# Kernel optimization log

Hardware: AMD Instinct MI355X
Metric: run time of the kernel (lower is better)

Reference implementation:

```python
import jax, jax.numpy as jnp
import numpy as np

N = 100_000      # nodes
E = 3_200_000    # directed edges (avg degree 32)
F_IN = 503
C = 32           # GATConv out_channels, heads=1
NEG_SLOPE = 0.2  # PyG GATConv default


def setup_inputs() -> dict:
    key = jax.random.key(0)
    ks = jax.random.split(key, 14)
    x = jax.random.normal(ks[0], (N, F_IN), jnp.float32)
    edge_index = jax.random.randint(ks[1], (2, E), 0, N)
    edge_weight = jax.random.uniform(ks[2], (E, 1), jnp.float32)
    input_mask = jnp.ones((N, 1), jnp.float32)
    # GATConv params (heads=1)
    W_src = jax.random.normal(ks[3], (C, F_IN), jnp.float32) * 0.02
    att_src = jax.random.normal(ks[4], (C,), jnp.float32) * 0.1
    att_dst = jax.random.normal(ks[5], (C,), jnp.float32) * 0.1
    att_edge = jax.random.normal(ks[6], (C,), jnp.float32) * 0.1
    W_edge = jax.random.normal(ks[7], (C, 1), jnp.float32) * 0.1
    bias_conv = jnp.zeros((C,), jnp.float32)
    # dense heads
    Wb = jax.random.normal(ks[8], (1, C), jnp.float32) * 0.1
    bb = jnp.zeros((1,), jnp.float32)
    Ww = jax.random.normal(ks[9], (1, C), jnp.float32) * 0.1
    bw = jnp.zeros((1,), jnp.float32)
    return {"x": x, "edge_index": edge_index, "edge_weight": edge_weight,
            "input_mask": input_mask, "W_src": W_src, "att_src": att_src,
            "att_dst": att_dst, "att_edge": att_edge, "W_edge": W_edge,
            "bias_conv": bias_conv, "Wb": Wb, "bb": bb, "Ww": Ww, "bw": bw}


def reference(x, edge_index, edge_weight, input_mask, W_src, att_src, att_dst,
              att_edge, W_edge, bias_conv, Wb, bb, Ww, bw):
    n = x.shape[0]
    xl = x @ W_src.T                       # [N, C] transformed node features
    a_src = xl @ att_src                   # [N] per-node source attention logit
    a_dst = xl @ att_dst                   # [N]
    src, dst = edge_index[0], edge_index[1]
    # add_self_loops=True with fill_value='mean' for edge_attr (PyG default)
    loop = jnp.arange(n)
    mean_attr = jnp.mean(edge_weight, axis=0, keepdims=True)      # [1,1]
    ea = jnp.concatenate([edge_weight, jnp.broadcast_to(mean_attr, (n, 1))], 0)
    s = jnp.concatenate([src, loop])       # [E+N]
    d = jnp.concatenate([dst, loop])
    a_edge = (ea @ W_edge.T) @ att_edge    # [E+N]
    alpha = jax.nn.leaky_relu(a_src[s] + a_dst[d] + a_edge, NEG_SLOPE)
    # softmax over incoming edges of each destination node
    amax = jax.ops.segment_max(alpha, d, num_segments=n)
    ex = jnp.exp(alpha - amax[d])
    denom = jax.ops.segment_sum(ex, d, num_segments=n)
    w = ex / denom[d]                      # [E+N] attention coeffs
    msg = xl[s] * w[:, None]               # [E+N, C]
    out = jax.ops.segment_sum(msg, d, num_segments=n) + bias_conv  # [N, C]
    h = jax.nn.relu(out)
    biases = (h @ Wb.T + bb) * input_mask  # [N, 1]
    weights = ((h[src] + h[dst]) * 0.5) @ Ww.T + bw  # [E, 1]
    return weights, biases
```

## Files before the change

kernel.cpp:

```cpp
#include <hip/hip_runtime.h>
#include <stdint.h>

#define NN 100000
#define NE 3200000
#define FIN 503
#define COUT 32
#define NSLOPE 0.2f

#define BSH 6
#define NB 1563
#define HB 256
#define EPB (NE / HB)
#define MAXBE 2400
#define NREG 10

typedef __bf16 bf16x8 __attribute__((ext_vector_type(8)));
typedef float  f32x4  __attribute__((ext_vector_type(4)));

__device__ __forceinline__ unsigned short bf1(float f) {
    unsigned u = __float_as_uint(f);
    u = (u + 0x7FFFu + ((u >> 16) & 1u)) >> 16;
    return (unsigned short)u;
}
__device__ __forceinline__ unsigned bf2(float a, float b) {
    return (unsigned)bf1(a) | ((unsigned)bf1(b) << 16);
}
__device__ __forceinline__ float unbf(unsigned short h) {
    return __uint_as_float(((unsigned)h) << 16);
}

__global__ __launch_bounds__(256)
void k_stats(const float* __restrict__ ew, float* __restrict__ partial,
             const float* __restrict__ W, uint4* __restrict__ wfrag)
{
    const int t = threadIdx.x;
    const int gid = blockIdx.x * 256 + t;

    if (gid < 2048) {
        int c = gid & 31;
        int quad = (gid >> 5) & 3;
        int chunk = gid >> 7;
        int kb = chunk * 32 + quad * 8;
        float v[8];
        #pragma unroll
        for (int j = 0; j < 8; ++j) {
            int k = kb + j;
            v[j] = (k < FIN) ? W[c * FIN + k] : 0.f;
        }
        uint4 o;
        o.x = bf2(v[0], v[1]); o.y = bf2(v[2], v[3]);
        o.z = bf2(v[4], v[5]); o.w = bf2(v[6], v[7]);
        wfrag[gid] = o;
    }

    const float4* ew4 = (const float4*)ew;
    float s = 0.f;
    for (int i = gid; i < NE / 4; i += gridDim.x * 256) {
        float4 v = ew4[i];
        s += v.x + v.y + v.z + v.w;
    }
    #pragma unroll
    for (int off = 32; off > 0; off >>= 1) s += __shfl_xor(s, off);
    __shared__ float wsum[4];
    if ((t & 63) == 0) wsum[t >> 6] = s;
    __syncthreads();
    if (t == 0) partial[blockIdx.x] = wsum[0] + wsum[1] + wsum[2] + wsum[3];
}

#define GR 64

__global__ __launch_bounds__(256)
void k_gemm(const float* __restrict__ x, const uint4* __restrict__ wfrag,
            const float* __restrict__ att_s, const float* __restrict__ att_d,
            unsigned short* __restrict__ xlb,
            float* __restrict__ a_src, float* __restrict__ a_dst)
{
    __shared__ __align__(16) float xs[GR][36];
    __shared__ __align__(16) unsigned short os[GR * 40];
    const int t = threadIdx.x;
    const int wv = t >> 6, lane = t & 63;
    const int m16 = lane & 15, quad = lane >> 4;
    const int row0 = blockIdx.x * GR;
    const int srow = t >> 5;
    const int scol = t & 31;

    f32x4 acc0 = {0.f, 0.f, 0.f, 0.f};
    f32x4 acc1 = {0.f, 0.f, 0.f, 0.f};
    const int rowf = wv * 16 + m16;

    for (int ch = 0; ch < 16; ++ch) {
        const int k = ch * 32 + scol;
        #pragma unroll
        for (int p = 0; p < 8; ++p) {
            int r = p * 8 + srow;
            int rg = row0 + r;
            rg = (rg < NN) ? rg : (NN - 1);
            xs[r][scol] = (k < FIN) ? x[(size_t)rg * FIN + k] : 0.f;
        }
        __syncthreads();
        float av[8];
        *(f32x4*)&av[0] = *(const f32x4*)&xs[rowf][quad * 8];
        *(f32x4*)&av[4] = *(const f32x4*)&xs[rowf][quad * 8 + 4];
        bf16x8 af;
        #pragma unroll
        for (int j = 0; j < 8; ++j) af[j] = (__bf16)av[j];
        uint4 b0 = wfrag[ch * 128 + quad * 32 + m16];
        uint4 b1 = wfrag[ch * 128 + quad * 32 + 16 + m16];
        acc0 = __builtin_amdgcn_mfma_f32_16x16x32_bf16(af, *(bf16x8*)&b0, acc0, 0, 0, 0);
        acc1 = __builtin_amdgcn_mfma_f32_16x16x32_bf16(af, *(bf16x8*)&b1, acc1, 0, 0, 0);
        __syncthreads();
    }

    #pragma unroll
    for (int r = 0; r < 4; ++r) {
        int rr = wv * 16 + quad * 4 + r;
        os[rr * 40 + m16]      = bf1(acc0[r]);
        os[rr * 40 + 16 + m16] = bf1(acc1[r]);
    }
    __syncthreads();
    {
        int r = t >> 2, c0 = (t & 3) * 8;
        int grow = row0 + r;
        uint4 o = *(const uint4*)&os[r * 40 + c0];
        float s = 0.f, dd = 0.f;
        const unsigned short* oh = (const unsigned short*)&o;
        #pragma unroll
        for (int j = 0; j < 8; ++j) {
            float v = unbf(oh[j]);
            s  += v * att_s[c0 + j];
            dd += v * att_d[c0 + j];
        }
        s  += __shfl_xor(s, 1, 4);  s  += __shfl_xor(s, 2, 4);
        dd += __shfl_xor(dd, 1, 4); dd += __shfl_xor(dd, 2, 4);
        if (grow < NN) {
            *(uint4*)&xlb[(size_t)grow * COUT + c0] = o;
            if ((t & 3) == 0) { a_src[grow] = s; a_dst[grow] = dd; }
        }
    }
}

__global__ __launch_bounds__(512)
void k_hist(const int* __restrict__ ei_dst, unsigned* __restrict__ part)
{
    __shared__ unsigned h[NB];
    for (int i = threadIdx.x; i < NB; i += 512) h[i] = 0u;
    __syncthreads();
    const int base = blockIdx.x * EPB;
    for (int i = threadIdx.x; i < EPB; i += 512)
        atomicAdd(&h[ei_dst[base + i] >> BSH], 1u);
    __syncthreads();
    for (int i = threadIdx.x; i < NB; i += 512)
        part[(size_t)blockIdx.x * NB + i] = h[i];
}

__global__ void k_colscan(unsigned* __restrict__ part, unsigned* __restrict__ colsum)
{
    __shared__ unsigned sm[HB];
    const int t = threadIdx.x;
    const int bkt = blockIdx.x;
    unsigned v = part[(size_t)t * NB + bkt];
    sm[t] = v;
    for (int off = 1; off < HB; off <<= 1) {
        __syncthreads();
        unsigned tv = (t >= off) ? sm[t - off] : 0u;
        __syncthreads();
        sm[t] += tv;
    }
    __syncthreads();
    part[(size_t)t * NB + bkt] = sm[t] - v;
    if (t == HB - 1) colsum[bkt] = sm[t];
}

__global__ void k_bscan(const unsigned* __restrict__ colsum, unsigned* __restrict__ bbase,
                        const float* __restrict__ partial, const float* __restrict__ W_edge,
                        const float* __restrict__ att_e, float* __restrict__ stats)
{
    const int t = threadIdx.x;
    {
        __shared__ float fs[256];
        float ps = partial[t] + partial[t + 256] + partial[t + 512] + partial[t + 768];
        fs[t] = ps;
        __syncthreads();
        for (int off = 128; off > 0; off >>= 1) {
            if (t < off) fs[t] += fs[t + off];
            __syncthreads();
        }
        if (t == 0) {
            stats[0] = fs[0];
            float k = 0.f;
            for (int c = 0; c < COUT; ++c) k += W_edge[c] * att_e[c];
            stats[1] = k;
        }
    }
    __syncthreads();

    __shared__ unsigned sm[256];
    __shared__ unsigned carry;
    if (t == 0) carry = 0u;
    __syncthreads();
    for (int c0 = 0; c0 < NB; c0 += 256) {
        int i = c0 + t;
        unsigned v = (i < NB) ? colsum[i] : 0u;
        sm[t] = v;
        for (int off = 1; off < 256; off <<= 1) {
            __syncthreads();
            unsigned tv = (t >= off) ? sm[t - off] : 0u;
            __syncthreads();
            sm[t] += tv;
        }
        __syncthreads();
        if (i < NB) bbase[i] = carry + sm[t] - v;
        __syncthreads();
        if (t == 0) carry += sm[255];
        __syncthreads();
    }
    if (t == 0) bbase[NB] = carry;
}

__global__ __launch_bounds__(512)
void k_scatter(const int* __restrict__ ei, const float* __restrict__ ew,
               const float* __restrict__ a_src, const float* __restrict__ stats,
               const unsigned* __restrict__ part, const unsigned* __restrict__ bbase,
               uint2* __restrict__ csr)
{
    __shared__ unsigned cur[NB];
    const int b = blockIdx.x;
    for (int i = threadIdx.x; i < NB; i += 512)
        cur[i] = bbase[i] + part[(size_t)b * NB + i];
    __syncthreads();
    const float kc = stats[1];
    const int base = b * EPB;
    for (int i = threadIdx.x; i < EPB; i += 512) {
        int e = base + i;
        int s = ei[e];
        int d = ei[NE + e];
        float pre = a_src[s] + kc * ew[e];
        unsigned pos = atomicAdd(&cur[d >> BSH], 1u);
        csr[pos] = make_uint2((unsigned)s | ((unsigned)(d & 63) << 20),
                              __float_as_uint(pre));
    }
}

__global__ __launch_bounds__(256)
void k_aggr(const uint2* __restrict__ csr, const unsigned* __restrict__ bbase,
            const float* __restrict__ a_src, const float* __restrict__ a_dst,
            const unsigned short* __restrict__ xlb, const float* __restrict__ stats,
            const float* __restrict__ bias_conv, const float* __restrict__ Wb,
            const float* __restrict__ bb, const float* __restrict__ Ww,
            const float* __restrict__ mask, float* __restrict__ out_b,
            float* __restrict__ hw)
{
    __shared__ uint2 rec[MAXBE];
    __shared__ unsigned seg[65], cur[64];
    const int t = threadIdx.x;
    const int b = blockIdx.x;
    const int jb = (int)bbase[b];
    int ne = (int)bbase[b + 1] - jb;
    if (ne > MAXBE) ne = MAXBE;

    uint2 rg[NREG];
    #pragma unroll
    for (int j = 0; j < NREG; ++j) {
        int i = t + j * 256;
        rg[j] = (i < ne) ? csr[jb + i] : make_uint2(0u, 0u);
    }
    if (t < 64) cur[t] = 0u;
    __syncthreads();
    #pragma unroll
    for (int j = 0; j < NREG; ++j)
        if (t + j * 256 < ne) atomicAdd(&cur[rg[j].x >> 20], 1u);
    __syncthreads();
    if (t < 64) {
        unsigned v = cur[t];
        unsigned s = v;
        #pragma unroll
        for (int off = 1; off < 64; off <<= 1) {
            unsigned u = __shfl_up(s, off, 64);
            if (t >= off) s += u;
        }
        seg[t + 1] = s;
        cur[t] = s - v;
        if (t == 0) seg[0] = 0u;
    }
    __syncthreads();
    #pragma unroll
    for (int j = 0; j < NREG; ++j)
        if (t + j * 256 < ne) {
            unsigned pos = atomicAdd(&cur[rg[j].x >> 20], 1u);
            rec[pos] = rg[j];
        }
    __syncthreads();

    const float kmean = stats[1] * (stats[0] * (1.f / NE));
    const int lane = t & 31;
    for (int dl = t >> 5; dl < 64; dl += 8) {
        int d = (b << BSH) + dl;
        if (d >= NN) continue;
        const float adv = a_dst[d];
        float a0 = a_src[d] + adv + kmean;
        a0 = (a0 > 0.f) ? a0 : NSLOPE * a0;
        const float ps = __expf(a0);
        float l = 0.f;
        float acc = ps * unbf(xlb[(size_t)d * COUT + lane]);
        const int j0 = (int)seg[dl], j1 = (int)seg[dl + 1];
        for (int tb = j0; tb < j1; tb += 32) {
            int j = tb + lane;
            float p = 0.f;
            if (j < j1) {
                uint2 en = rec[j];
                float a = __uint_as_float(en.y) + adv;
                a = (a > 0.f) ? a : NSLOPE * a;
                p = __expf(a);
                rec[j].y = __float_as_uint(p);
            }
            l += p;
            int cnte = min(32, j1 - tb);
            #pragma unroll 4
            for (int k = 0; k < cnte; ++k) {
                uint2 en = rec[tb + k];
                acc += __uint_as_float(en.y) *
                       unbf(xlb[(size_t)(en.x & 0xFFFFFu) * COUT + lane]);
            }
        }
        #pragma unroll
        for (int off = 16; off > 0; off >>= 1) l += __shfl_xor(l, off, 32);
        l += ps;
        float h = fmaxf(acc / l + bias_conv[lane], 0.f);
        float pb = h * Wb[lane];
        float pw = h * Ww[lane];
        #pragma unroll
        for (int off = 16; off > 0; off >>= 1) {
            pb += __shfl_xor(pb, off, 32);
            pw += __shfl_xor(pw, off, 32);
        }
        if (lane == 0) {
            out_b[d] = (pb + bb[0]) * mask[d];
            hw[d] = pw;
        }
    }
}

__global__ void k_weights(const int* __restrict__ ei, const float* __restrict__ hw,
                          const float* __restrict__ bw, float* __restrict__ out_w)
{
    int e4 = blockIdx.x * 256 + threadIdx.x;
    if (e4 < NE / 4) {
        int4 s4 = ((const int4*)ei)[e4];
        int4 d4 = ((const int4*)(ei + NE))[e4];
        float bwv = bw[0];
        float4 o;
        o.x = 0.5f * (hw[s4.x] + hw[d4.x]) + bwv;
        o.y = 0.5f * (hw[s4.y] + hw[d4.y]) + bwv;
        o.z = 0.5f * (hw[s4.z] + hw[d4.z]) + bwv;
        o.w = 0.5f * (hw[s4.w] + hw[d4.w]) + bwv;
        ((float4*)out_w)[e4] = o;
    }
}

extern "C" void kernel_launch(void* const* d_in, const int* in_sizes, int n_in,
                              void* d_out, int out_size, void* d_ws, size_t ws_size,
                              hipStream_t stream)
{
    const float* x        = (const float*)d_in[0];
    const int*   ei       = (const int*)d_in[1];
    const float* ew       = (const float*)d_in[2];
    const float* mask     = (const float*)d_in[3];
    const float* W_src    = (const float*)d_in[4];
    const float* att_src  = (const float*)d_in[5];
    const float* att_dst  = (const float*)d_in[6];
    const float* att_edge = (const float*)d_in[7];
    const float* W_edge   = (const float*)d_in[8];
    const float* bias_c   = (const float*)d_in[9];
    const float* Wb       = (const float*)d_in[10];
    const float* bb       = (const float*)d_in[11];
    const float* Ww       = (const float*)d_in[12];
    const float* bw       = (const float*)d_in[13];
    (void)in_sizes; (void)n_in; (void)out_size; (void)ws_size;

    char* wsp = (char*)d_ws;
    size_t off = 0;
    auto alloc = [&](size_t bytes) -> void* {
        void* p = wsp + off;
        off = (off + bytes + 255) & ~(size_t)255;
        return p;
    };
    unsigned short* xlb    = (unsigned short*)alloc((size_t)NN * COUT * 2);
    uint4*    wfrag  = (uint4*)alloc(2048 * 16);
    float*    a_src  = (float*)alloc((size_t)NN * 4);
    float*    a_dst  = (float*)alloc((size_t)NN * 4);
    float*    stats  = (float*)alloc(256);
    float*    partial= (float*)alloc(1024 * 4);
    unsigned* part   = (unsigned*)alloc((size_t)HB * NB * 4);
    unsigned* colsum = (unsigned*)alloc((size_t)NB * 4);
    unsigned* bbase  = (unsigned*)alloc((size_t)(NB + 1) * 4);
    uint2*    csr    = (uint2*)alloc((size_t)NE * 8);
    float*    hw     = (float*)alloc((size_t)NN * 4);

    float* out_w = (float*)d_out;
    float* out_b = out_w + NE;

    k_stats   <<<1024, 256, 0, stream>>>(ew, partial, W_src, wfrag);
    k_gemm    <<<(NN + GR - 1) / GR, 256, 0, stream>>>(x, wfrag, att_src, att_dst,
                                                       xlb, a_src, a_dst);
    k_hist    <<<HB, 512, 0, stream>>>(ei + NE, part);
    k_colscan <<<NB, HB, 0, stream>>>(part, colsum);
    k_bscan   <<<1, 256, 0, stream>>>(colsum, bbase, partial, W_edge, att_edge, stats);
    k_scatter <<<HB, 512, 0, stream>>>(ei, ew, a_src, stats, part, bbase, csr);
    k_aggr    <<<NB, 256, 0, stream>>>(csr, bbase, a_src, a_dst, xlb, stats,
                                       bias_c, Wb, bb, Ww, mask, out_b, hw);
    k_weights <<<NE / 4 / 256, 256, 0, stream>>>(ei, hw, bw, out_w);
}
```

Baseline: 530.0 us.

## Fuse edge-weight stats and dst histogram kernels, enlarge GEMM row tile

Merges the edge-weight sum / W fragment packing kernel with the destination-bucket histogram kernel into one 256-block launch, removing a kernel launch and a pass boundary. It also doubles the GEMM row tile to 128 rows with 512-thread blocks, halving the block count while keeping per-wave MFMA work the same. The partial-sum buffer shrinks to 256 entries to match. GEMM shared arrays appear to be sized by GR, so the larger tile raises LDS use per block and could lower occupancy.

```diff
diff --git a/kernel.cpp b/kernel.cpp
--- a/kernel.cpp
+++ b/kernel.cpp
@@ -29,12 +29,18 @@
     return __uint_as_float(((unsigned)h) << 16);
 }
 
-__global__ __launch_bounds__(256)
-void k_stats(const float* __restrict__ ew, float* __restrict__ partial,
-             const float* __restrict__ W, uint4* __restrict__ wfrag)
-{
+__global__ __launch_bounds__(512)
+void k_pre(const int* __restrict__ ei_dst, const float* __restrict__ ew,
+           const float* __restrict__ W, uint4* __restrict__ wfrag,
+           float* __restrict__ partial, unsigned* __restrict__ part)
+{
+    __shared__ unsigned h[NB];
+    __shared__ float wsum[8];
     const int t = threadIdx.x;
-    const int gid = blockIdx.x * 256 + t;
+    const int b = blockIdx.x;
+    const int gid = b * 512 + t;
+
+    for (int i = t; i < NB; i += 512) h[i] = 0u;
 
     if (gid < 2048) {
         int c = gid & 31;
@@ -52,24 +58,35 @@
         o.z = bf2(v[4], v[5]); o.w = bf2(v[6], v[7]);
         wfrag[gid] = o;
     }
+    __syncthreads();
+
+    const int base = b * EPB;
+    for (int i = t; i < EPB; i += 512)
+        atomicAdd(&h[ei_dst[base + i] >> BSH], 1u);
 
     const float4* ew4 = (const float4*)ew;
     float s = 0.f;
-    for (int i = gid; i < NE / 4; i += gridDim.x * 256) {
+    for (int i = gid; i < NE / 4; i += HB * 512) {
         float4 v = ew4[i];
         s += v.x + v.y + v.z + v.w;
     }
     #pragma unroll
     for (int off = 32; off > 0; off >>= 1) s += __shfl_xor(s, off);
-    __shared__ float wsum[4];
     if ((t & 63) == 0) wsum[t >> 6] = s;
     __syncthreads();
-    if (t == 0) partial[blockIdx.x] = wsum[0] + wsum[1] + wsum[2] + wsum[3];
-}
-
-#define GR 64
-
-__global__ __launch_bounds__(256)
+    if (t == 0) {
+        float ss = 0.f;
+        #pragma unroll
+        for (int j = 0; j < 8; ++j) ss += wsum[j];
+        partial[b] = ss;
+    }
+    for (int i = t; i < NB; i += 512)
+        part[(size_t)b * NB + i] = h[i];
+}
+
+#define GR 128
+
+__global__ __launch_bounds__(512)
 void k_gemm(const float* __restrict__ x, const uint4* __restrict__ wfrag,
             const float* __restrict__ att_s, const float* __restrict__ att_d,
             unsigned short* __restrict__ xlb,
@@ -92,7 +109,7 @@
         const int k = ch * 32 + scol;
         #pragma unroll
         for (int p = 0; p < 8; ++p) {
-            int r = p * 8 + srow;
+            int r = p * 16 + srow;
             int rg = row0 + r;
             rg = (rg < NN) ? rg : (NN - 1);
             xs[r][scol] = (k < FIN) ? x[(size_t)rg * FIN + k] : 0.f;
@@ -139,20 +156,6 @@
     }
 }
 
-__global__ __launch_bounds__(512)
-void k_hist(const int* __restrict__ ei_dst, unsigned* __restrict__ part)
-{
-    __shared__ unsigned h[NB];
-    for (int i = threadIdx.x; i < NB; i += 512) h[i] = 0u;
-    __syncthreads();
-    const int base = blockIdx.x * EPB;
-    for (int i = threadIdx.x; i < EPB; i += 512)
-        atomicAdd(&h[ei_dst[base + i] >> BSH], 1u);
-    __syncthreads();
-    for (int i = threadIdx.x; i < NB; i += 512)
-        part[(size_t)blockIdx.x * NB + i] = h[i];
-}
-
 __global__ void k_colscan(unsigned* __restrict__ part, unsigned* __restrict__ colsum)
 {
     __shared__ unsigned sm[HB];
@@ -178,8 +181,7 @@
     const int t = threadIdx.x;
     {
         __shared__ float fs[256];
-        float ps = partial[t] + partial[t + 256] + partial[t + 512] + partial[t + 768];
-        fs[t] = ps;
+        fs[t] = partial[t];
         __syncthreads();
         for (int off = 128; off > 0; off >>= 1) {
             if (t < off) fs[t] += fs[t + off];
@@ -389,7 +391,7 @@
     float*    a_src  = (float*)alloc((size_t)NN * 4);
     float*    a_dst  = (float*)alloc((size_t)NN * 4);
     float*    stats  = (float*)alloc(256);
-    float*    partial= (float*)alloc(1024 * 4);
+    float*    partial= (float*)alloc((size_t)HB * 4);
     unsigned* part   = (unsigned*)alloc((size_t)HB * NB * 4);
     unsigned* colsum = (unsigned*)alloc((size_t)NB * 4);
     unsigned* bbase  = (unsigned*)alloc((size_t)(NB + 1) * 4);
@@ -399,10 +401,9 @@
     float* out_w = (float*)d_out;
     float* out_b = out_w + NE;
 
-    k_stats   <<<1024, 256, 0, stream>>>(ew, partial, W_src, wfrag);
-    k_gemm    <<<(NN + GR - 1) / GR, 256, 0, stream>>>(x, wfrag, att_src, att_dst,
+    k_pre     <<<HB, 512, 0, stream>>>(ei + NE, ew, W_src, wfrag, partial, part);
+    k_gemm    <<<(NN + GR - 1) / GR, 512, 0, stream>>>(x, wfrag, att_src, att_dst,
                                                        xlb, a_src, a_dst);
-    k_hist    <<<HB, 512, 0, stream>>>(ei + NE, part);
     k_colscan <<<NB, HB, 0, stream>>>(part, colsum);
     k_bscan   <<<1, 256, 0, stream>>>(colsum, bbase, partial, W_edge, att_edge, stats);
     k_scatter <<<HB, 512, 0, stream>>>(ei, ew, a_src, stats, part, bbase, csr);
```

New measurement: 536.4 us. No clear change (+1.2%).
